# Optimization experiments

Hardware: AMD Instinct MI355X
Metric: run time of the kernel (lower is better)

## Reference

```python
import jax, jax.numpy as jnp
import numpy as np

NEG_SLOPE = 0.2

def gat_conv(x, src, dst, W, a_src, a_dst, b, n_nodes):
    # x: [N, Fin] -> h: [N, Fout]; edges (src->dst) incl. self-loops
    h = x @ W                                   # [N, Fout]
    as_ = h @ a_src                             # [N] per-node source score
    ad_ = h @ a_dst                             # [N] per-node dest score
    e = jax.nn.leaky_relu(as_[src] + ad_[dst], NEG_SLOPE)   # [E]
    # segment softmax over edges sharing the same destination
    e_max = jax.ops.segment_max(e, dst, num_segments=n_nodes)
    e_exp = jnp.exp(e - e_max[dst])
    e_sum = jax.ops.segment_sum(e_exp, dst, num_segments=n_nodes)
    alpha = e_exp / (e_sum[dst] + 1e-16)        # [E]
    out = jax.ops.segment_sum(alpha[:, None] * h[src], dst, num_segments=n_nodes)
    return out + b

def setup_inputs() -> dict:
    key = jax.random.key(0)
    ks = jax.random.split(key, 12)
    N, E, Fin, H = 100000, 3200000, 128, 32
    def g(k, shape, scale):
        return jax.random.normal(k, shape, dtype=jnp.float32) * scale
    return {
        "x": g(ks[0], (N, Fin), 1.0),
        "edge_index": jax.random.randint(ks[1], (2, E), 0, N, dtype=jnp.int32),
        "W1": g(ks[2], (Fin, H), 1.0 / np.sqrt(Fin)),
        "att_src1": g(ks[3], (H,), 1.0 / np.sqrt(H)),
        "att_dst1": g(ks[4], (H,), 1.0 / np.sqrt(H)),
        "b1": jnp.zeros((H,), jnp.float32),
        "W2": g(ks[5], (H, H), 1.0 / np.sqrt(H)),
        "att_src2": g(ks[6], (H,), 1.0 / np.sqrt(H)),
        "att_dst2": g(ks[7], (H,), 1.0 / np.sqrt(H)),
        "b2": jnp.zeros((H,), jnp.float32),
        "Wf": g(ks[8], (H, H), 1.0 / np.sqrt(H)),
        "bf": jnp.zeros((H,), jnp.float32),
    }

def reference(x, edge_index, W1, att_src1, att_dst1, b1, W2, att_src2, att_dst2, b2, Wf, bf):
    n_nodes = x.shape[0]
    loops = jnp.arange(n_nodes, dtype=edge_index.dtype)
    src = jnp.concatenate([edge_index[0], loops])  # add_self_loops=True (PyG default)
    dst = jnp.concatenate([edge_index[1], loops])
    h = jax.nn.relu(gat_conv(x, src, dst, W1, att_src1, att_dst1, b1, n_nodes))
    h = jax.nn.relu(gat_conv(h, src, dst, W2, att_src2, att_dst2, b2, n_nodes))
    return h @ Wf + bf
```

## Files before the change

### kernel.cpp

```cpp
#include <hip/hip_runtime.h>

#define NEG_SLOPE 0.2f
#define BK_SH 8
#define BK_SZ 256
#define MAXBUCK 512
#define EPB 8192

typedef _Float16 half8 __attribute__((ext_vector_type(8)));
typedef float f32x4 __attribute__((ext_vector_type(4)));

__global__ __launch_bounds__(256) void k_castx(const float* __restrict__ x,
                                               _Float16* __restrict__ xh,
                                               int n8) {
  int i = blockIdx.x * 256 + threadIdx.x;
  if (i >= n8) return;
  const float4* p = reinterpret_cast<const float4*>(x) + 2 * (size_t)i;
  float4 v0 = p[0], v1 = p[1];
  half8 h;
  h[0] = (_Float16)v0.x; h[1] = (_Float16)v0.y;
  h[2] = (_Float16)v0.z; h[3] = (_Float16)v0.w;
  h[4] = (_Float16)v1.x; h[5] = (_Float16)v1.y;
  h[6] = (_Float16)v1.z; h[7] = (_Float16)v1.w;
  *(reinterpret_cast<half8*>(xh) + i) = h;
}

__global__ __launch_bounds__(256) void k_castW(const float* __restrict__ W,
                                               _Float16* __restrict__ Wt) {
  for (int i = threadIdx.x; i < 128 * 32; i += 256) {
    int k = i >> 5, f = i & 31;
    Wt[f * 128 + k] = (_Float16)W[i];
  }
}

__global__ __launch_bounds__(256) void k_feat_mfma(
    const _Float16* __restrict__ xh, const _Float16* __restrict__ Wt,
    const float* __restrict__ a_src, const float* __restrict__ a_dst,
    _Float16* __restrict__ Hh, float* __restrict__ as_, float* __restrict__ ad_,
    int N) {
  int w = threadIdx.x >> 6;
  int lane = threadIdx.x & 63;
  int base = (blockIdx.x * 4 + w) * 16;
  if (base >= N) return;
  int row16 = lane & 15;
  int kg = lane >> 4;
  f32x4 acc0 = {0.f, 0.f, 0.f, 0.f};
  f32x4 acc1 = {0.f, 0.f, 0.f, 0.f};
  const half8* xa =
      reinterpret_cast<const half8*>(xh + (size_t)(base + row16) * 128 + kg * 8);
#pragma unroll
  for (int kt = 0; kt < 4; ++kt) {
    half8 a = xa[kt * 4];
    half8 b0 = *reinterpret_cast<const half8*>(Wt + (size_t)row16 * 128 +
                                               kt * 32 + kg * 8);
    half8 b1 = *reinterpret_cast<const half8*>(Wt + (size_t)(16 + row16) * 128 +
                                               kt * 32 + kg * 8);
    acc0 = __builtin_amdgcn_mfma_f32_16x16x32_f16(a, b0, acc0, 0, 0, 0);
    acc1 = __builtin_amdgcn_mfma_f32_16x16x32_f16(a, b1, acc1, 0, 0, 0);
  }
  float aS0 = a_src[row16], aS1 = a_src[16 + row16];
  float aD0 = a_dst[row16], aD1 = a_dst[16 + row16];
  float tS[4], tD[4];
#pragma unroll
  for (int r = 0; r < 4; ++r) {
    int row = base + kg * 4 + r;
    Hh[(size_t)row * 32 + row16] = (_Float16)acc0[r];
    Hh[(size_t)row * 32 + 16 + row16] = (_Float16)acc1[r];
    tS[r] = acc0[r] * aS0 + acc1[r] * aS1;
    tD[r] = acc0[r] * aD0 + acc1[r] * aD1;
  }
#pragma unroll
  for (int off = 1; off <= 8; off <<= 1) {
#pragma unroll
    for (int r = 0; r < 4; ++r) {
      tS[r] += __shfl_xor(tS[r], off, 64);
      tD[r] += __shfl_xor(tD[r], off, 64);
    }
  }
  if (row16 == 0) {
#pragma unroll
    for (int r = 0; r < 4; ++r) {
      as_[base + kg * 4 + r] = tS[r];
      ad_[base + kg * 4 + r] = tD[r];
    }
  }
}

__global__ __launch_bounds__(256) void k_feat32(
    const float* __restrict__ X, const float* __restrict__ W,
    const float* __restrict__ a_src, const float* __restrict__ a_dst,
    _Float16* __restrict__ Hh, float* __restrict__ as_, float* __restrict__ ad_,
    int N) {
  __shared__ float sW[32 * 32];
  __shared__ float sX[8][32];
  for (int i = threadIdx.x; i < 32 * 32; i += 256) sW[i] = W[i];
  int node0 = blockIdx.x * 8;
  {
    int i = threadIdx.x;
    int n = node0 + (i >> 5);
    sX[i >> 5][i & 31] = (n < N) ? X[(size_t)n * 32 + (i & 31)] : 0.f;
  }
  __syncthreads();
  int g = threadIdx.x >> 5;
  int f = threadIdx.x & 31;
  int n = node0 + g;
  if (n >= N) return;
  float acc = 0.f;
#pragma unroll
  for (int k = 0; k < 32; ++k) acc += sX[g][k] * sW[k * 32 + f];
  Hh[(size_t)n * 32 + f] = (_Float16)acc;
  float vs = acc * a_src[f];
  float vd = acc * a_dst[f];
#pragma unroll
  for (int off = 16; off; off >>= 1) {
    vs += __shfl_down(vs, off, 32);
    vd += __shfl_down(vd, off, 32);
  }
  if (f == 0) {
    as_[n] = vs;
    ad_[n] = vd;
  }
}

__global__ __launch_bounds__(256) void k_zero(int* __restrict__ p, int n) {
  int i = blockIdx.x * 256 + threadIdx.x;
  if (i < n) p[i] = 0;
}

__global__ __launch_bounds__(256) void k_bhist(const int* __restrict__ ei,
                                               int E, int* __restrict__ bcnt,
                                               int nbuck) {
  __shared__ int h[MAXBUCK];
  for (int i = threadIdx.x; i < nbuck; i += 256) h[i] = 0;
  __syncthreads();
  long base = (long)blockIdx.x * EPB;
#pragma unroll 4
  for (int i = 0; i < EPB / 256; ++i) {
    long e = base + i * 256 + threadIdx.x;
    if (e < E) atomicAdd(&h[ei[E + e] >> BK_SH], 1);
  }
  __syncthreads();
  for (int i = threadIdx.x; i < nbuck; i += 256)
    if (h[i]) atomicAdd(&bcnt[i], h[i]);
}

__global__ __launch_bounds__(1024) void k_scan(const int* __restrict__ bcnt,
                                               int* __restrict__ boff,
                                               int* __restrict__ bcur,
                                               int* __restrict__ ptr, int nbuck,
                                               int N, int E) {
  __shared__ int s[1024];
  int t = threadIdx.x;
  int v = (t < nbuck) ? bcnt[t] : 0;
  s[t] = v;
  __syncthreads();
  for (int off = 1; off < 1024; off <<= 1) {
    int x = (t >= off) ? s[t - off] : 0;
    __syncthreads();
    s[t] += x;
    __syncthreads();
  }
  if (t < nbuck) {
    boff[t] = s[t] - v;
    bcur[t] = s[t] - v;
  }
  if (t == 0) {
    boff[nbuck] = E;
    ptr[N] = E;
  }
}

__global__ __launch_bounds__(256) void k_binA(const int* __restrict__ ei, int E,
                                              int* __restrict__ bcur,
                                              unsigned* __restrict__ packed,
                                              int nbuck) {
  __shared__ int h[MAXBUCK];
  __shared__ int lbase[MAXBUCK];
  __shared__ int lb[MAXBUCK];
  __shared__ int cur[MAXBUCK];
  __shared__ int psum[256];
  __shared__ unsigned rec[EPB];
  __shared__ unsigned short bkt[EPB];
  int t = threadIdx.x;
  for (int i = t; i < MAXBUCK; i += 256) h[i] = 0;
  __syncthreads();
  long base = (long)blockIdx.x * EPB;
  int cnt = (int)((E - base) < EPB ? (E - base) : EPB);
#pragma unroll 4
  for (int i = 0; i < EPB / 256; ++i) {
    int e = i * 256 + t;
    if (e < cnt) atomicAdd(&h[ei[E + base + e] >> BK_SH], 1);
  }
  __syncthreads();
  for (int i = t; i < nbuck; i += 256)
    lbase[i] = h[i] ? atomicAdd(&bcur[i], h[i]) : 0;
  int a0 = h[2 * t], a1 = h[2 * t + 1];
  psum[t] = a0 + a1;
  __syncthreads();
  for (int off = 1; off < 256; off <<= 1) {
    int x = (t >= off) ? psum[t - off] : 0;
    __syncthreads();
    psum[t] += x;
    __syncthreads();
  }
  int pex = psum[t] - (a0 + a1);
  lb[2 * t] = pex;
  lb[2 * t + 1] = pex + a0;
  cur[2 * t] = pex;
  cur[2 * t + 1] = pex + a0;
  __syncthreads();
#pragma unroll 4
  for (int i = 0; i < EPB / 256; ++i) {
    int e = i * 256 + t;
    if (e < cnt) {
      int s = ei[base + e], d = ei[E + base + e];
      int b = d >> BK_SH;
      int pos = atomicAdd(&cur[b], 1);
      rec[pos] = ((unsigned)s << 8) | (unsigned)(d & (BK_SZ - 1));
      bkt[pos] = (unsigned short)b;
    }
  }
  __syncthreads();
  for (int i = t; i < cnt; i += 256) {
    int b = bkt[i];
    packed[(size_t)lbase[b] + (i - lb[b])] = rec[i];
  }
}

__global__ __launch_bounds__(256) void k_binB(const unsigned* __restrict__ packed,
                                              const int* __restrict__ boff,
                                              int* __restrict__ ptr,
                                              int* __restrict__ srcs, int N) {
  int b = blockIdx.x;
  int beg = boff[b], end = boff[b + 1];
  int t = threadIdx.x;
  __shared__ int lcnt[BK_SZ];
  __shared__ int sc[BK_SZ];
  __shared__ int lcur[BK_SZ];
  lcnt[t] = 0;
  __syncthreads();
  for (int i = beg + t; i < end; i += 256)
    atomicAdd(&lcnt[packed[i] & (BK_SZ - 1)], 1);
  __syncthreads();
  int v = lcnt[t];
  sc[t] = v;
  __syncthreads();
  for (int off = 1; off < 256; off <<= 1) {
    int x = (t >= off) ? sc[t - off] : 0;
    __syncthreads();
    sc[t] += x;
    __syncthreads();
  }
  int excl = sc[t] - v;
  int node = (b << BK_SH) + t;
  if (node < N) ptr[node] = beg + excl;
  lcur[t] = excl;
  __syncthreads();
  for (int i = beg + t; i < end; i += 256) {
    unsigned p = packed[i];
    int slot = atomicAdd(&lcur[p & (BK_SZ - 1)], 1);
    srcs[(size_t)beg + slot] = (int)(p >> 8);
  }
}

template <int FINAL>
__global__ __launch_bounds__(256) void k_gatherT(
    const int* __restrict__ ptr, const int* __restrict__ srcs,
    const _Float16* __restrict__ Hh, const float* __restrict__ as_,
    const float* __restrict__ ad_, const float* __restrict__ b,
    const float* __restrict__ Wf, const float* __restrict__ bf,
    float* __restrict__ OUT, int N) {
  __shared__ float sWf[32 * 32];
  __shared__ float sO[8][33];
  if (FINAL) {
    for (int i = threadIdx.x; i < 32 * 32; i += 256) sWf[i] = Wf[i];
  }
  int g = threadIdx.x >> 5;
  int lane = threadIdx.x & 31;
  int sub = lane >> 2;
  int q = lane & 3;
  int d = blockIdx.x * 8 + g;
  int dc = d < N ? d : N - 1;
  float ad_d = ad_[dc];
  float acc[8] = {0.f, 0.f, 0.f, 0.f, 0.f, 0.f, 0.f, 0.f};
  float sumw = 0.f;
  int beg = ptr[dc], end = ptr[dc + 1];
  int j = beg;
  bool v0 = sub < end - j;
  int sid0 = v0 ? srcs[j + sub] : dc;
  float sa0 = as_[sid0];
  half8 hv0 = *reinterpret_cast<const half8*>(Hh + (size_t)sid0 * 32 + q * 8);
  while (j < end) {
    int jn = j + 8;
    bool v1 = sub < end - jn;
    int sid1 = v1 ? srcs[jn + sub] : dc;
    float sa1 = as_[sid1];
    half8 hv1 = *reinterpret_cast<const half8*>(Hh + (size_t)sid1 * 32 + q * 8);
    float sc2 = sa0 + ad_d;
    float el = sc2 > 0.f ? sc2 : NEG_SLOPE * sc2;
    float w = v0 ? __expf(el) : 0.f;
#pragma unroll
    for (int i = 0; i < 8; ++i) acc[i] += w * (float)hv0[i];
    sumw += w;
    j = jn; v0 = v1; sid0 = sid1; sa0 = sa1; hv0 = hv1;
  }
#pragma unroll
  for (int off = 4; off <= 16; off <<= 1) {
#pragma unroll
    for (int i = 0; i < 8; ++i) acc[i] += __shfl_xor(acc[i], off, 32);
    sumw += __shfl_xor(sumw, off, 32);
  }
  if (sub == 0) {
    float s0 = as_[dc] + ad_d;
    float e0 = s0 > 0.f ? s0 : NEG_SLOPE * s0;
    float w0 = __expf(e0);
    half8 hs = *reinterpret_cast<const half8*>(Hh + (size_t)dc * 32 + q * 8);
#pragma unroll
    for (int i = 0; i < 8; ++i) acc[i] += w0 * (float)hs[i];
    sumw += w0;
    float inv = 1.f / (sumw + 1e-16f);
    if (FINAL) {
#pragma unroll
      for (int i = 0; i < 8; ++i)
        sO[g][q * 8 + i] = fmaxf(acc[i] * inv + b[q * 8 + i], 0.f);
    } else if (d < N) {
      f32x4 o1, o2;
#pragma unroll
      for (int i = 0; i < 4; ++i) {
        o1[i] = fmaxf(acc[i] * inv + b[q * 8 + i], 0.f);
        o2[i] = fmaxf(acc[4 + i] * inv + b[q * 8 + 4 + i], 0.f);
      }
      *reinterpret_cast<f32x4*>(OUT + (size_t)d * 32 + q * 8) = o1;
      *reinterpret_cast<f32x4*>(OUT + (size_t)d * 32 + q * 8 + 4) = o2;
    }
  }
  if (FINAL) {
    __syncthreads();
    float accf = bf[lane];
#pragma unroll
    for (int k = 0; k < 32; ++k) accf += sO[g][k] * sWf[k * 32 + lane];
    if (d < N) OUT[(size_t)d * 32 + lane] = accf;
  }
}

extern "C" void kernel_launch(void* const* d_in, const int* in_sizes, int n_in,
                              void* d_out, int out_size, void* d_ws,
                              size_t ws_size, hipStream_t stream) {
  const float* x = (const float*)d_in[0];
  const int* ei = (const int*)d_in[1];
  const float* W1 = (const float*)d_in[2];
  const float* as1 = (const float*)d_in[3];
  const float* ad1 = (const float*)d_in[4];
  const float* b1 = (const float*)d_in[5];
  const float* W2 = (const float*)d_in[6];
  const float* as2 = (const float*)d_in[7];
  const float* ad2 = (const float*)d_in[8];
  const float* b2 = (const float*)d_in[9];
  const float* Wf = (const float*)d_in[10];
  const float* bf = (const float*)d_in[11];
  float* out = (float*)d_out;

  const int H = in_sizes[3];
  const int FIN = in_sizes[2] / H;
  const int N = in_sizes[0] / FIN;
  const int E = in_sizes[1] / 2;
  const int nbuck = (N + BK_SZ - 1) >> BK_SH;
  (void)n_in; (void)out_size; (void)ws_size; (void)H;

  size_t r0 = (size_t)E * 4;
  size_t xhB = (size_t)N * FIN * 2;
  size_t bfB = (size_t)N * 32 * 4;
  if (xhB > r0) r0 = xhB;
  if (bfB > r0) r0 = bfB;
  char* basep = (char*)d_ws;
  unsigned* packed = (unsigned*)basep;
  _Float16* xh = (_Float16*)basep;
  float* Bf = (float*)basep;
  char* p = basep + r0;
  _Float16* Hh = (_Float16*)p;  p += (size_t)N * 32 * 2;
  _Float16* Wt = (_Float16*)p;  p += (size_t)128 * 32 * 2;
  float* asv = (float*)p;       p += (size_t)N * 4;
  float* adv = (float*)p;       p += (size_t)N * 4;
  int* ptr = (int*)p;           p += (size_t)(N + 1) * 4;
  int* srcs = (int*)p;          p += (size_t)E * 4;
  int* bcnt = (int*)p;          p += (size_t)nbuck * 4;
  int* boff = (int*)p;          p += (size_t)(nbuck + 1) * 4;
  int* bcur = (int*)p;

  const int nodeBlocks = (N + 7) / 8;
  const int binBlocks = (E + EPB - 1) / EPB;
  const int mfmaBlocks = (N / 16 + 3) / 4;

  k_zero<<<(nbuck + 255) / 256, 256, 0, stream>>>(bcnt, nbuck);
  k_bhist<<<binBlocks, 256, 0, stream>>>(ei, E, bcnt, nbuck);
  k_scan<<<1, 1024, 0, stream>>>(bcnt, boff, bcur, ptr, nbuck, N, E);
  k_binA<<<binBlocks, 256, 0, stream>>>(ei, E, bcur, packed, nbuck);
  k_binB<<<nbuck, 256, 0, stream>>>(packed, boff, ptr, srcs, N);

  k_castx<<<(N * FIN / 8 + 255) / 256, 256, 0, stream>>>(x, xh, N * FIN / 8);
  k_castW<<<1, 256, 0, stream>>>(W1, Wt);
  k_feat_mfma<<<mfmaBlocks, 256, 0, stream>>>(xh, Wt, as1, ad1, Hh, asv, adv, N);
  k_gatherT<0><<<nodeBlocks, 256, 0, stream>>>(ptr, srcs, Hh, asv, adv, b1,
                                               nullptr, nullptr, Bf, N);

  k_feat32<<<nodeBlocks, 256, 0, stream>>>(Bf, W2, as2, ad2, Hh, asv, adv, N);
  k_gatherT<1><<<nodeBlocks, 256, 0, stream>>>(ptr, srcs, Hh, asv, adv, b2, Wf,
                                               bf, out, N);
}
```

Measured before the change: 236.0 us.

## Fuse x cast into MFMA feature kernel, fp16 layer-2 path, deeper gather prefetch

The separate fp32-to-fp16 cast pass over x is folded into the first feature kernel, which now loads fp32 rows and converts them in registers. The layer-1 output is stored as fp16 instead of fp32, and layer 2's feature transform now uses an MFMA kernel over that fp16 buffer with a transposed fp16 W2. The gather loop prefetches two edge groups ahead instead of one. Together these cut a full kernel launch and memory traffic for intermediates, at the cost of extra fp16 rounding of the hidden activations and more live registers in the gather loop.

```diff
diff --git a/kernel.cpp b/kernel.cpp
--- a/kernel.cpp
+++ b/kernel.cpp
@@ -9,31 +9,17 @@
 typedef _Float16 half8 __attribute__((ext_vector_type(8)));
 typedef float f32x4 __attribute__((ext_vector_type(4)));
 
-__global__ __launch_bounds__(256) void k_castx(const float* __restrict__ x,
-                                               _Float16* __restrict__ xh,
-                                               int n8) {
-  int i = blockIdx.x * 256 + threadIdx.x;
-  if (i >= n8) return;
-  const float4* p = reinterpret_cast<const float4*>(x) + 2 * (size_t)i;
-  float4 v0 = p[0], v1 = p[1];
-  half8 h;
-  h[0] = (_Float16)v0.x; h[1] = (_Float16)v0.y;
-  h[2] = (_Float16)v0.z; h[3] = (_Float16)v0.w;
-  h[4] = (_Float16)v1.x; h[5] = (_Float16)v1.y;
-  h[6] = (_Float16)v1.z; h[7] = (_Float16)v1.w;
-  *(reinterpret_cast<half8*>(xh) + i) = h;
-}
-
 __global__ __launch_bounds__(256) void k_castW(const float* __restrict__ W,
-                                               _Float16* __restrict__ Wt) {
-  for (int i = threadIdx.x; i < 128 * 32; i += 256) {
+                                               _Float16* __restrict__ Wt,
+                                               int K) {
+  for (int i = threadIdx.x; i < K * 32; i += 256) {
     int k = i >> 5, f = i & 31;
-    Wt[f * 128 + k] = (_Float16)W[i];
-  }
-}
-
-__global__ __launch_bounds__(256) void k_feat_mfma(
-    const _Float16* __restrict__ xh, const _Float16* __restrict__ Wt,
+    Wt[f * K + k] = (_Float16)W[i];
+  }
+}
+
+__global__ __launch_bounds__(256) void k_feat1(
+    const float* __restrict__ x, const _Float16* __restrict__ Wt,
     const float* __restrict__ a_src, const float* __restrict__ a_dst,
     _Float16* __restrict__ Hh, float* __restrict__ as_, float* __restrict__ ad_,
     int N) {
@@ -45,11 +31,16 @@
   int kg = lane >> 4;
   f32x4 acc0 = {0.f, 0.f, 0.f, 0.f};
   f32x4 acc1 = {0.f, 0.f, 0.f, 0.f};
-  const half8* xa =
-      reinterpret_cast<const half8*>(xh + (size_t)(base + row16) * 128 + kg * 8);
+  const float* xr = x + (size_t)(base + row16) * 128 + kg * 8;
 #pragma unroll
   for (int kt = 0; kt < 4; ++kt) {
-    half8 a = xa[kt * 4];
+    float4 u0 = *reinterpret_cast<const float4*>(xr + kt * 32);
+    float4 u1 = *reinterpret_cast<const float4*>(xr + kt * 32 + 4);
+    half8 a;
+    a[0] = (_Float16)u0.x; a[1] = (_Float16)u0.y;
+    a[2] = (_Float16)u0.z; a[3] = (_Float16)u0.w;
+    a[4] = (_Float16)u1.x; a[5] = (_Float16)u1.y;
+    a[6] = (_Float16)u1.z; a[7] = (_Float16)u1.w;
     half8 b0 = *reinterpret_cast<const half8*>(Wt + (size_t)row16 * 128 +
                                                kt * 32 + kg * 8);
     half8 b1 = *reinterpret_cast<const half8*>(Wt + (size_t)(16 + row16) * 128 +
@@ -85,39 +76,52 @@
   }
 }
 
-__global__ __launch_bounds__(256) void k_feat32(
-    const float* __restrict__ X, const float* __restrict__ W,
+__global__ __launch_bounds__(256) void k_feat2(
+    const _Float16* __restrict__ Bh, const _Float16* __restrict__ Wt,
     const float* __restrict__ a_src, const float* __restrict__ a_dst,
     _Float16* __restrict__ Hh, float* __restrict__ as_, float* __restrict__ ad_,
     int N) {
-  __shared__ float sW[32 * 32];
-  __shared__ float sX[8][32];
-  for (int i = threadIdx.x; i < 32 * 32; i += 256) sW[i] = W[i];
-  int node0 = blockIdx.x * 8;
-  {
-    int i = threadIdx.x;
-    int n = node0 + (i >> 5);
-    sX[i >> 5][i & 31] = (n < N) ? X[(size_t)n * 32 + (i & 31)] : 0.f;
-  }
-  __syncthreads();
-  int g = threadIdx.x >> 5;
-  int f = threadIdx.x & 31;
-  int n = node0 + g;
-  if (n >= N) return;
-  float acc = 0.f;
-#pragma unroll
-  for (int k = 0; k < 32; ++k) acc += sX[g][k] * sW[k * 32 + f];
-  Hh[(size_t)n * 32 + f] = (_Float16)acc;
-  float vs = acc * a_src[f];
-  float vd = acc * a_dst[f];
-#pragma unroll
-  for (int off = 16; off; off >>= 1) {
-    vs += __shfl_down(vs, off, 32);
-    vd += __shfl_down(vd, off, 32);
-  }
-  if (f == 0) {
-    as_[n] = vs;
-    ad_[n] = vd;
+  int w = threadIdx.x >> 6;
+  int lane = threadIdx.x & 63;
+  int base = (blockIdx.x * 4 + w) * 16;
+  if (base >= N) return;
+  int row16 = lane & 15;
+  int kg = lane >> 4;
+  half8 a = *reinterpret_cast<const half8*>(Bh + (size_t)(base + row16) * 32 +
+                                            kg * 8);
+  half8 b0 =
+      *reinterpret_cast<const half8*>(Wt + (size_t)row16 * 32 + kg * 8);
+  half8 b1 =
+      *reinterpret_cast<const half8*>(Wt + (size_t)(16 + row16) * 32 + kg * 8);
+  f32x4 acc0 = {0.f, 0.f, 0.f, 0.f};
+  f32x4 acc1 = {0.f, 0.f, 0.f, 0.f};
+  acc0 = __builtin_amdgcn_mfma_f32_16x16x32_f16(a, b0, acc0, 0, 0, 0);
+  acc1 = __builtin_amdgcn_mfma_f32_16x16x32_f16(a, b1, acc1, 0, 0, 0);
+  float aS0 = a_src[row16], aS1 = a_src[16 + row16];
+  float aD0 = a_dst[row16], aD1 = a_dst[16 + row16];
+  float tS[4], tD[4];
+#pragma unroll
+  for (int r = 0; r < 4; ++r) {
+    int row = base + kg * 4 + r;
+    Hh[(size_t)row * 32 + row16] = (_Float16)acc0[r];
+    Hh[(size_t)row * 32 + 16 + row16] = (_Float16)acc1[r];
+    tS[r] = acc0[r] * aS0 + acc1[r] * aS1;
+    tD[r] = acc0[r] * aD0 + acc1[r] * aD1;
+  }
+#pragma unroll
+  for (int off = 1; off <= 8; off <<= 1) {
+#pragma unroll
+    for (int r = 0; r < 4; ++r) {
+      tS[r] += __shfl_xor(tS[r], off, 64);
+      tD[r] += __shfl_xor(tD[r], off, 64);
+    }
+  }
+  if (row16 == 0) {
+#pragma unroll
+    for (int r = 0; r < 4; ++r) {
+      as_[base + kg * 4 + r] = tS[r];
+      ad_[base + kg * 4 + r] = tD[r];
+    }
   }
 }
 
@@ -268,7 +272,7 @@
     const _Float16* __restrict__ Hh, const float* __restrict__ as_,
     const float* __restrict__ ad_, const float* __restrict__ b,
     const float* __restrict__ Wf, const float* __restrict__ bf,
-    float* __restrict__ OUT, int N) {
+    void* __restrict__ OUTv, int N) {
   __shared__ float sWf[32 * 32];
   __shared__ float sO[8][33];
   if (FINAL) {
@@ -284,24 +288,28 @@
   float acc[8] = {0.f, 0.f, 0.f, 0.f, 0.f, 0.f, 0.f, 0.f};
   float sumw = 0.f;
   int beg = ptr[dc], end = ptr[dc + 1];
-  int j = beg;
-  bool v0 = sub < end - j;
-  int sid0 = v0 ? srcs[j + sub] : dc;
+  bool v0 = sub < end - beg;
+  int sid0 = v0 ? srcs[beg + sub] : dc;
   float sa0 = as_[sid0];
   half8 hv0 = *reinterpret_cast<const half8*>(Hh + (size_t)sid0 * 32 + q * 8);
-  while (j < end) {
-    int jn = j + 8;
-    bool v1 = sub < end - jn;
-    int sid1 = v1 ? srcs[jn + sub] : dc;
-    float sa1 = as_[sid1];
-    half8 hv1 = *reinterpret_cast<const half8*>(Hh + (size_t)sid1 * 32 + q * 8);
+  bool v1 = sub < end - (beg + 8);
+  int sid1 = v1 ? srcs[beg + 8 + sub] : dc;
+  float sa1 = as_[sid1];
+  half8 hv1 = *reinterpret_cast<const half8*>(Hh + (size_t)sid1 * 32 + q * 8);
+  for (int j = beg; j < end; j += 8) {
+    int jn = j + 16;
+    bool v2 = sub < end - jn;
+    int sid2 = v2 ? srcs[jn + sub] : dc;
+    float sa2 = as_[sid2];
+    half8 hv2 = *reinterpret_cast<const half8*>(Hh + (size_t)sid2 * 32 + q * 8);
     float sc2 = sa0 + ad_d;
     float el = sc2 > 0.f ? sc2 : NEG_SLOPE * sc2;
     float w = v0 ? __expf(el) : 0.f;
 #pragma unroll
     for (int i = 0; i < 8; ++i) acc[i] += w * (float)hv0[i];
     sumw += w;
-    j = jn; v0 = v1; sid0 = sid1; sa0 = sa1; hv0 = hv1;
+    v0 = v1; sid0 = sid1; sa0 = sa1; hv0 = hv1;
+    v1 = v2; sid1 = sid2; sa1 = sa2; hv1 = hv2;
   }
 #pragma unroll
   for (int off = 4; off <= 16; off <<= 1) {
@@ -323,14 +331,11 @@
       for (int i = 0; i < 8; ++i)
         sO[g][q * 8 + i] = fmaxf(acc[i] * inv + b[q * 8 + i], 0.f);
     } else if (d < N) {
-      f32x4 o1, o2;
-#pragma unroll
-      for (int i = 0; i < 4; ++i) {
-        o1[i] = fmaxf(acc[i] * inv + b[q * 8 + i], 0.f);
-        o2[i] = fmaxf(acc[4 + i] * inv + b[q * 8 + 4 + i], 0.f);
-      }
-      *reinterpret_cast<f32x4*>(OUT + (size_t)d * 32 + q * 8) = o1;
-      *reinterpret_cast<f32x4*>(OUT + (size_t)d * 32 + q * 8 + 4) = o2;
+      half8 o;
+#pragma unroll
+      for (int i = 0; i < 8; ++i)
+        o[i] = (_Float16)fmaxf(acc[i] * inv + b[q * 8 + i], 0.f);
+      *reinterpret_cast<half8*>((_Float16*)OUTv + (size_t)d * 32 + q * 8) = o;
     }
   }
   if (FINAL) {
@@ -338,7 +343,7 @@
     float accf = bf[lane];
 #pragma unroll
     for (int k = 0; k < 32; ++k) accf += sO[g][k] * sWf[k * 32 + lane];
-    if (d < N) OUT[(size_t)d * 32 + lane] = accf;
+    if (d < N) ((float*)OUTv)[(size_t)d * 32 + lane] = accf;
   }
 }
 
@@ -367,23 +372,21 @@
   (void)n_in; (void)out_size; (void)ws_size; (void)H;
 
   size_t r0 = (size_t)E * 4;
-  size_t xhB = (size_t)N * FIN * 2;
-  size_t bfB = (size_t)N * 32 * 4;
-  if (xhB > r0) r0 = xhB;
-  if (bfB > r0) r0 = bfB;
+  size_t bhB = (size_t)N * 32 * 2;
+  if (bhB > r0) r0 = bhB;
   char* basep = (char*)d_ws;
   unsigned* packed = (unsigned*)basep;
-  _Float16* xh = (_Float16*)basep;
-  float* Bf = (float*)basep;
+  _Float16* Bh = (_Float16*)basep;
   char* p = basep + r0;
-  _Float16* Hh = (_Float16*)p;  p += (size_t)N * 32 * 2;
-  _Float16* Wt = (_Float16*)p;  p += (size_t)128 * 32 * 2;
-  float* asv = (float*)p;       p += (size_t)N * 4;
-  float* adv = (float*)p;       p += (size_t)N * 4;
-  int* ptr = (int*)p;           p += (size_t)(N + 1) * 4;
-  int* srcs = (int*)p;          p += (size_t)E * 4;
-  int* bcnt = (int*)p;          p += (size_t)nbuck * 4;
-  int* boff = (int*)p;          p += (size_t)(nbuck + 1) * 4;
+  _Float16* Hh = (_Float16*)p;   p += (size_t)N * 32 * 2;
+  _Float16* Wt1 = (_Float16*)p;  p += (size_t)128 * 32 * 2;
+  _Float16* Wt2 = (_Float16*)p;  p += (size_t)32 * 32 * 2;
+  float* asv = (float*)p;        p += (size_t)N * 4;
+  float* adv = (float*)p;        p += (size_t)N * 4;
+  int* ptr = (int*)p;            p += (size_t)(N + 1) * 4;
+  int* srcs = (int*)p;           p += (size_t)E * 4;
+  int* bcnt = (int*)p;           p += (size_t)nbuck * 4;
+  int* boff = (int*)p;           p += (size_t)(nbuck + 1) * 4;
   int* bcur = (int*)p;
 
   const int nodeBlocks = (N + 7) / 8;
@@ -396,13 +399,14 @@
   k_binA<<<binBlocks, 256, 0, stream>>>(ei, E, bcur, packed, nbuck);
   k_binB<<<nbuck, 256, 0, stream>>>(packed, boff, ptr, srcs, N);
 
-  k_castx<<<(N * FIN / 8 + 255) / 256, 256, 0, stream>>>(x, xh, N * FIN / 8);
-  k_castW<<<1, 256, 0, stream>>>(W1, Wt);
-  k_feat_mfma<<<mfmaBlocks, 256, 0, stream>>>(xh, Wt, as1, ad1, Hh, asv, adv, N);
+  k_castW<<<1, 256, 0, stream>>>(W1, Wt1, 128);
+  k_castW<<<1, 256, 0, stream>>>(W2, Wt2, 32);
+
+  k_feat1<<<mfmaBlocks, 256, 0, stream>>>(x, Wt1, as1, ad1, Hh, asv, adv, N);
   k_gatherT<0><<<nodeBlocks, 256, 0, stream>>>(ptr, srcs, Hh, asv, adv, b1,
-                                               nullptr, nullptr, Bf, N);
-
-  k_feat32<<<nodeBlocks, 256, 0, stream>>>(Bf, W2, as2, ad2, Hh, asv, adv, N);
+                                               nullptr, nullptr, Bh, N);
+
+  k_feat2<<<mfmaBlocks, 256, 0, stream>>>(Bh, Wt2, as2, ad2, Hh, asv, adv, N);
   k_gatherT<1><<<nodeBlocks, 256, 0, stream>>>(ptr, srcs, Hh, asv, adv, b2, Wf,
                                                bf, out, N);
 }
```

New measurement: 220.2 us. 1.07x faster.
